# Kernel tuning notes

Hardware: AMD Instinct MI355X
Metric: run time of the kernel (lower is better)

Reference implementation:

```python
import jax, jax.numpy as jnp
import numpy as np

NUM_HEADS = 8


def setup_inputs() -> dict:
    key = jax.random.key(0)
    ks = jax.random.split(key, 5)
    b, c, h, w = 8, 256, 32, 32
    x = jax.random.normal(ks[0], (b, c, h, w), dtype=jnp.float32)
    w_qkv = jax.random.normal(ks[1], (3 * c, c), dtype=jnp.float32) * (c ** -0.5)
    b_qkv = jax.random.normal(ks[2], (3 * c,), dtype=jnp.float32) * 0.02
    w_proj = jax.random.normal(ks[3], (c, c), dtype=jnp.float32) * (c ** -0.5)
    b_proj = jax.random.normal(ks[4], (c,), dtype=jnp.float32) * 0.02
    return {"x": x, "w_qkv": w_qkv, "b_qkv": b_qkv, "w_proj": w_proj, "b_proj": b_proj}


def reference(x, w_qkv, b_qkv, w_proj, b_proj):
    b, c, h, w = x.shape
    nh = NUM_HEADS
    dh = c // nh
    L = h * w
    scale = dh ** -0.5
    # 1x1 conv == per-pixel GEMM
    qkv = jnp.einsum('bchw,oc->bohw', x, w_qkv) + b_qkv[None, :, None, None]
    qkv = qkv.reshape(b, 3, nh, dh, L)
    q, k, v = qkv[:, 0], qkv[:, 1], qkv[:, 2]  # each (b, nh, dh, L)
    attn = jnp.einsum('bhdi,bhdj->bhij', q, k) * scale  # (b, nh, L, L)
    attn = jax.nn.softmax(attn, axis=-1)
    out = jnp.einsum('bhdj,bhij->bhdi', v, attn)  # (b, nh, dh, L)
    out = out.reshape(b, c, h, w)
    proj = jnp.einsum('bchw,oc->bohw', out, w_proj) + b_proj[None, :, None, None]
    return x + proj
```

## Files before the change

kernel.cpp:

```cpp
#include <hip/hip_runtime.h>
#include <math.h>

#define B_   8
#define CIN  256
#define L_   1024
#define NH_  8
#define DH_  32

typedef __attribute__((ext_vector_type(8))) short short8;
typedef __attribute__((ext_vector_type(4))) short short4v;
typedef __attribute__((ext_vector_type(4))) float f32x4;
typedef __attribute__((ext_vector_type(4))) unsigned int uint4v;
typedef __attribute__((ext_vector_type(2))) unsigned int uint2v;

__device__ inline short f2bf_hu(float f) {
    union { float f; unsigned u; } v; v.f = f;
    return (short)((v.u + 0x8000u) >> 16);
}
__device__ inline unsigned pkbf2(float a, float b) {
    union { float f; unsigned u; } x, y; x.f = a; y.f = b;
    return __builtin_amdgcn_perm(y.u + 0x8000u, x.u + 0x8000u, 0x07060302u);
}

__global__ __launch_bounds__(256) void qkv_gemm(
    const float* __restrict__ x, const float* __restrict__ w,
    const float* __restrict__ bias, short* __restrict__ qkvT)
{
    __shared__ short Xs[64][40];
    __shared__ short Wt[128][40];
    const int t = threadIdx.x, lane = t & 63, wv = t >> 6;
    const int n = lane & 15, quad = lane >> 4;
    const int b = blockIdx.z, o0 = blockIdx.y * 128, l0 = blockIdx.x * 64;

    float bias_r[8];
    #pragma unroll
    for (int nf = 0; nf < 8; nf++) bias_r[nf] = bias[o0 + nf * 16 + n];

    f32x4 acc[8];
    #pragma unroll
    for (int nf = 0; nf < 8; nf++) acc[nf] = (f32x4){0.f, 0.f, 0.f, 0.f};

    const int cS = t >> 3, lsS = (t & 7) * 8;

    for (int c0 = 0; c0 < CIN; c0 += 32) {
        {
            const float* xp = &x[(((size_t)b * CIN + c0 + cS) << 10) + l0 + lsS];
            const float4 xa = *(const float4*)xp;
            const float4 xb = *(const float4*)(xp + 4);
            const float vals[8] = {xa.x, xa.y, xa.z, xa.w, xb.x, xb.y, xb.z, xb.w};
            #pragma unroll
            for (int k = 0; k < 8; k++) {
                const int l = lsS + k;
                const int col = (((cS >> 3) ^ (l & 3)) << 3) | (cS & 7);
                Xs[l][col] = f2bf_hu(vals[k]);
            }
        }
        {
            const int o = t >> 1, cs = (t & 1) * 16;
            const float* wp = &w[(size_t)(o0 + o) * CIN + c0 + cs];
            const float4 w0 = *(const float4*)(wp);
            const float4 w1 = *(const float4*)(wp + 4);
            const float4 w2 = *(const float4*)(wp + 8);
            const float4 w3 = *(const float4*)(wp + 12);
            uint4v pa = { pkbf2(w0.x, w0.y), pkbf2(w0.z, w0.w),
                          pkbf2(w1.x, w1.y), pkbf2(w1.z, w1.w) };
            uint4v pb = { pkbf2(w2.x, w2.y), pkbf2(w2.z, w2.w),
                          pkbf2(w3.x, w3.y), pkbf2(w3.z, w3.w) };
            *(uint4v*)&Wt[o][cs]     = pa;
            *(uint4v*)&Wt[o][cs + 8] = pb;
        }
        __syncthreads();

        const int arow = wv * 16 + n;
        const short8 af = *(const short8*)&Xs[arow][(quad ^ (arow & 3)) * 8];
        #pragma unroll
        for (int nf = 0; nf < 8; nf++) {
            const short8 bf = *(const short8*)&Wt[nf * 16 + n][quad * 8];
            acc[nf] = __builtin_amdgcn_mfma_f32_16x16x32_bf16(af, bf, acc[nf], 0, 0, 0);
        }
        __syncthreads();
    }

    #pragma unroll
    for (int reg = 0; reg < 4; reg++) {
        const size_t l = l0 + wv * 16 + quad * 4 + reg;
        short* row = qkvT + (((size_t)b << 10) + l) * 768 + o0 + n;
        #pragma unroll
        for (int nf = 0; nf < 8; nf++)
            row[nf * 16] = f2bf_hu(acc[nf][reg] + bias_r[nf]);
    }
}

__global__ __launch_bounds__(256) void proj_gemm(
    const short* __restrict__ aT, const float* __restrict__ w,
    const float* __restrict__ bias, const float* __restrict__ resid,
    float* __restrict__ out)
{
    __shared__ short Xs[64][40];
    __shared__ short Wt[64][40];
    const int t = threadIdx.x, lane = t & 63, wv = t >> 6;
    const int n = lane & 15, quad = lane >> 4;
    const int b = blockIdx.z, o0 = blockIdx.y * 64, l0 = blockIdx.x * 64;

    float bias_r[4];
    #pragma unroll
    for (int reg = 0; reg < 4; reg++) bias_r[reg] = bias[o0 + wv * 16 + quad * 4 + reg];

    f32x4 acc[4];
    #pragma unroll
    for (int nf = 0; nf < 4; nf++) acc[nf] = (f32x4){0.f, 0.f, 0.f, 0.f};

    for (int c0 = 0; c0 < CIN; c0 += 32) {
        {
            const int l = t >> 2, cs = (t & 3) * 8;
            *(uint4v*)&Xs[l][cs] =
                *(const uint4v*)&aT[(((size_t)b << 10) + l0 + l) * CIN + c0 + cs];
        }
        {
            const int o = t >> 2, cs = (t & 3) * 8;
            const float* wp = &w[(size_t)(o0 + o) * CIN + c0 + cs];
            const float4 a4 = *(const float4*)(wp);
            const float4 b4 = *(const float4*)(wp + 4);
            uint4v pw = { pkbf2(a4.x, a4.y), pkbf2(a4.z, a4.w),
                          pkbf2(b4.x, b4.y), pkbf2(b4.z, b4.w) };
            *(uint4v*)&Wt[o][cs] = pw;
        }
        __syncthreads();

        const short8 af = *(const short8*)&Wt[wv * 16 + n][quad * 8];
        #pragma unroll
        for (int nf = 0; nf < 4; nf++) {
            const short8 bf = *(const short8*)&Xs[nf * 16 + n][quad * 8];
            acc[nf] = __builtin_amdgcn_mfma_f32_16x16x32_bf16(af, bf, acc[nf], 0, 0, 0);
        }
        __syncthreads();
    }

    #pragma unroll
    for (int reg = 0; reg < 4; reg++) {
        const int o = o0 + wv * 16 + quad * 4 + reg;
        #pragma unroll
        for (int nf = 0; nf < 4; nf++) {
            const size_t off = (((size_t)b * CIN + o) << 10) + l0 + nf * 16 + n;
            out[off] = acc[nf][reg] + bias_r[reg] + resid[off];
        }
    }
}

__global__ __launch_bounds__(256) void attn_mfma(
    const short* __restrict__ qkvT, short* __restrict__ attnoT)
{
    __shared__ short Vt[2][32][80];
    __shared__ __align__(16) char umem[64 * 80 * 2];
    short (*Ss)[80] = (short(*)[80])umem;
    float (*OtT)[38] = (float(*)[38])umem;

    const int t = threadIdx.x, lane = t & 63, wv = t >> 6;
    const int n = lane & 15, quad = lane >> 4;
    const int id = blockIdx.x;
    const int bh = id & 63;
    const int b = bh >> 3, h = bh & 7;
    const int i0 = (id >> 6) * 64;

    const short* base = qkvT + ((size_t)b << 10) * 768;

    const short8 qa = *(const short8*)&base[(size_t)(i0 + wv * 16 + n) * 768 + h * DH_ + quad * 8];

    short8 vf2;
    {
        const short one = (n == 0) ? (short)0x3F80 : (short)0;
        #pragma unroll
        for (int u = 0; u < 8; u++) vf2[u] = one;
    }

    f32x4 o_acc[3];
    #pragma unroll
    for (int nf = 0; nf < 3; nf++) o_acc[nf] = (f32x4){0.f, 0.f, 0.f, 0.f};

    const float K1 = 0.25503510f;
    const float K2 = 11.54156036f;
    const int TSTRIDE = 64 * 768;

    const short* kp0 = base + 256 + h * DH_ + (size_t)(0 * 16 + n) * 768 + quad * 8;
    const short* kp1 = kp0 + 16 * 768;
    const short* kp2 = kp0 + 32 * 768;
    const short* kp3 = kp0 + 48 * 768;
    const int jS = t >> 3, dsS = (t & 7) * 4;
    const short* vp0 = base + 512 + h * DH_ + (size_t)jS * 768 + dsS;
    const short* vp1 = vp0 + 32 * 768;

    const int vmsk = ((dsS >> 2) & 7) << 3;
    const int vwo0 = dsS * 80 + (jS ^ vmsk);
    const int vwo1 = dsS * 80 + ((jS + 32) ^ vmsk);
    short* const vtb0 = &Vt[0][0][0];
    short* const vtb1 = &Vt[1][0][0];
    short* const ssw  = &Ss[wv * 16 + n][quad * 4];
    const short* const ssr = &Ss[wv * 16 + n][quad * 8];
    int vro[2][2];
    #pragma unroll
    for (int nf = 0; nf < 2; nf++) {
        const int dv = nf * 16 + n;
        const int msk = ((dv >> 2) & 7) << 3;
        #pragma unroll
        for (int kk = 0; kk < 2; kk++)
            vro[kk][nf] = dv * 80 + ((kk * 32 + quad * 8) ^ msk);
    }

    short8 kfA[4], kfB[4];

    auto stageV = [&](short* vtb) {
        const short4v a = *(const short4v*)vp0; vp0 += TSTRIDE;
        const short4v c = *(const short4v*)vp1; vp1 += TSTRIDE;
        #pragma unroll
        for (int u = 0; u < 4; u++) {
            vtb[vwo0 + u * 80] = a[u];
            vtb[vwo1 + u * 80] = c[u];
        }
    };
    auto loadK = [&](short8* kf) {
        kf[0] = *(const short8*)kp0; kp0 += TSTRIDE;
        kf[1] = *(const short8*)kp1; kp1 += TSTRIDE;
        kf[2] = *(const short8*)kp2; kp2 += TSTRIDE;
        kf[3] = *(const short8*)kp3; kp3 += TSTRIDE;
    };
    auto tile = [&](const short8* kf, const short* vtb) {
        #pragma unroll
        for (int f = 0; f < 4; f++) {
            f32x4 z = {0.f, 0.f, 0.f, 0.f};
            const f32x4 sv = __builtin_amdgcn_mfma_f32_16x16x32_bf16(kf[f], qa, z, 0, 0, 0);
            const float p0 = __builtin_amdgcn_exp2f(fmaf(sv[0], K1, -K2));
            const float p1 = __builtin_amdgcn_exp2f(fmaf(sv[1], K1, -K2));
            const float p2 = __builtin_amdgcn_exp2f(fmaf(sv[2], K1, -K2));
            const float p3 = __builtin_amdgcn_exp2f(fmaf(sv[3], K1, -K2));
            uint2v pk = { pkbf2(p0, p1), pkbf2(p2, p3) };
            *(uint2v*)(ssw + f * 16) = pk;
        }
        #pragma unroll
        for (int kk = 0; kk < 2; kk++) {
            const short8 pf = *(const short8*)(ssr + kk * 32);
            #pragma unroll
            for (int nf = 0; nf < 2; nf++) {
                const short8 vf = *(const short8*)(vtb + vro[kk][nf]);
                o_acc[nf] = __builtin_amdgcn_mfma_f32_16x16x32_bf16(pf, vf, o_acc[nf], 0, 0, 0);
            }
            o_acc[2] = __builtin_amdgcn_mfma_f32_16x16x32_bf16(pf, vf2, o_acc[2], 0, 0, 0);
        }
    };

    stageV(vtb0);
    loadK(kfA);

    for (int itp = 0; itp < 8; itp++) {
        __syncthreads();
        stageV(vtb1);
        loadK(kfB);
        tile(kfA, vtb0);
        __syncthreads();
        if (itp < 7) { stageV(vtb0); loadK(kfA); }
        tile(kfB, vtb1);
    }

    __syncthreads();
    #pragma unroll
    for (int r = 0; r < 4; r++) {
        const float lv  = __shfl(o_acc[2][r], lane & 48, 64);
        const float inv = 1.f / lv;
        const int il = wv * 16 + quad * 4 + r;
        OtT[il][n]      = o_acc[0][r] * inv;
        OtT[il][16 + n] = o_acc[1][r] * inv;
    }
    __syncthreads();
    short* ob = attnoT + (((size_t)b << 10) + i0) * CIN + h * DH_;
    #pragma unroll
    for (int r = 0; r < 2; r++) {
        const int idx = t + r * 256;
        const int l = idx >> 3, cs = (idx & 7) * 4;
        uint2v pv;
        pv.x = pkbf2(OtT[l][cs],     OtT[l][cs + 1]);
        pv.y = pkbf2(OtT[l][cs + 2], OtT[l][cs + 3]);
        *(uint2v*)&ob[(size_t)l * CIN + cs] = pv;
    }
}

extern "C" void kernel_launch(void* const* d_in, const int* in_sizes, int n_in,
                              void* d_out, int out_size, void* d_ws, size_t ws_size,
                              hipStream_t stream) {
    const float* x      = (const float*)d_in[0];
    const float* w_qkv  = (const float*)d_in[1];
    const float* b_qkv  = (const float*)d_in[2];
    const float* w_proj = (const float*)d_in[3];
    const float* b_proj = (const float*)d_in[4];
    float* out = (float*)d_out;

    short* qkvT   = (short*)d_ws;
    short* attnoT = qkvT + (size_t)B_ * L_ * 768;

    qkv_gemm<<<dim3(16, 6, B_), 256, 0, stream>>>(x, w_qkv, b_qkv, qkvT);
    attn_mfma<<<dim3(1024), 256, 0, stream>>>(qkvT, attnoT);
    proj_gemm<<<dim3(16, 4, B_), 256, 0, stream>>>(attnoT, w_proj, b_proj, x, out);
}
```

Baseline: 127.5 us.

## Process two query sub-tiles per wave in attention to reuse K/V tiles

Each attention block now covers 128 query rows instead of 64: every wave holds two Q fragments and two sets of output accumulators, and the grid is halved to 512 blocks. Each K fragment loaded from global memory and each V tile staged in LDS now feeds twice as many MFMAs, so K/V traffic and staging cost per query are halved. The Ss buffer grows with a padded row stride of 88. The trade-off is higher register and LDS use per block and fewer blocks, which may reduce occupancy and the ability to hide latency on a 256-CU device.

```diff
diff --git a/kernel.cpp b/kernel.cpp
--- a/kernel.cpp
+++ b/kernel.cpp
@@ -151,8 +151,8 @@
     const short* __restrict__ qkvT, short* __restrict__ attnoT)
 {
     __shared__ short Vt[2][32][80];
-    __shared__ __align__(16) char umem[64 * 80 * 2];
-    short (*Ss)[80] = (short(*)[80])umem;
+    __shared__ __align__(16) char umem[128 * 88 * 2];
+    short (*Ss)[88] = (short(*)[88])umem;
     float (*OtT)[38] = (float(*)[38])umem;
 
     const int t = threadIdx.x, lane = t & 63, wv = t >> 6;
@@ -160,11 +160,15 @@
     const int id = blockIdx.x;
     const int bh = id & 63;
     const int b = bh >> 3, h = bh & 7;
-    const int i0 = (id >> 6) * 64;
+    const int i0 = (id >> 6) * 128;
 
     const short* base = qkvT + ((size_t)b << 10) * 768;
 
-    const short8 qa = *(const short8*)&base[(size_t)(i0 + wv * 16 + n) * 768 + h * DH_ + quad * 8];
+    short8 qa[2];
+    #pragma unroll
+    for (int a = 0; a < 2; a++)
+        qa[a] = *(const short8*)&base[(size_t)(i0 + wv * 32 + a * 16 + n) * 768
+                                      + h * DH_ + quad * 8];
 
     short8 vf2;
     {
@@ -173,15 +177,17 @@
         for (int u = 0; u < 8; u++) vf2[u] = one;
     }
 
-    f32x4 o_acc[3];
-    #pragma unroll
-    for (int nf = 0; nf < 3; nf++) o_acc[nf] = (f32x4){0.f, 0.f, 0.f, 0.f};
+    f32x4 o_acc[2][3];
+    #pragma unroll
+    for (int a = 0; a < 2; a++)
+        #pragma unroll
+        for (int nf = 0; nf < 3; nf++) o_acc[a][nf] = (f32x4){0.f, 0.f, 0.f, 0.f};
 
     const float K1 = 0.25503510f;
     const float K2 = 11.54156036f;
     const int TSTRIDE = 64 * 768;
 
-    const short* kp0 = base + 256 + h * DH_ + (size_t)(0 * 16 + n) * 768 + quad * 8;
+    const short* kp0 = base + 256 + h * DH_ + (size_t)n * 768 + quad * 8;
     const short* kp1 = kp0 + 16 * 768;
     const short* kp2 = kp0 + 32 * 768;
     const short* kp3 = kp0 + 48 * 768;
@@ -194,8 +200,8 @@
     const int vwo1 = dsS * 80 + ((jS + 32) ^ vmsk);
     short* const vtb0 = &Vt[0][0][0];
     short* const vtb1 = &Vt[1][0][0];
-    short* const ssw  = &Ss[wv * 16 + n][quad * 4];
-    const short* const ssr = &Ss[wv * 16 + n][quad * 8];
+    short* const ssw  = &Ss[wv * 32 + n][quad * 4];
+    const short* const ssr = &Ss[wv * 32 + n][quad * 8];
     int vro[2][2];
     #pragma unroll
     for (int nf = 0; nf < 2; nf++) {
@@ -226,24 +232,34 @@
     auto tile = [&](const short8* kf, const short* vtb) {
         #pragma unroll
         for (int f = 0; f < 4; f++) {
-            f32x4 z = {0.f, 0.f, 0.f, 0.f};
-            const f32x4 sv = __builtin_amdgcn_mfma_f32_16x16x32_bf16(kf[f], qa, z, 0, 0, 0);
-            const float p0 = __builtin_amdgcn_exp2f(fmaf(sv[0], K1, -K2));
-            const float p1 = __builtin_amdgcn_exp2f(fmaf(sv[1], K1, -K2));
-            const float p2 = __builtin_amdgcn_exp2f(fmaf(sv[2], K1, -K2));
-            const float p3 = __builtin_amdgcn_exp2f(fmaf(sv[3], K1, -K2));
-            uint2v pk = { pkbf2(p0, p1), pkbf2(p2, p3) };
-            *(uint2v*)(ssw + f * 16) = pk;
+            #pragma unroll
+            for (int a = 0; a < 2; a++) {
+                f32x4 z = {0.f, 0.f, 0.f, 0.f};
+                const f32x4 sv = __builtin_amdgcn_mfma_f32_16x16x32_bf16(kf[f], qa[a], z, 0, 0, 0);
+                const float p0 = __builtin_amdgcn_exp2f(fmaf(sv[0], K1, -K2));
+                const float p1 = __builtin_amdgcn_exp2f(fmaf(sv[1], K1, -K2));
+                const float p2 = __builtin_amdgcn_exp2f(fmaf(sv[2], K1, -K2));
+                const float p3 = __builtin_amdgcn_exp2f(fmaf(sv[3], K1, -K2));
+                uint2v pk = { pkbf2(p0, p1), pkbf2(p2, p3) };
+                *(uint2v*)(ssw + a * 16 * 88 + f * 16) = pk;
+            }
         }
         #pragma unroll
         for (int kk = 0; kk < 2; kk++) {
-            const short8 pf = *(const short8*)(ssr + kk * 32);
+            short8 pf[2];
+            #pragma unroll
+            for (int a = 0; a < 2; a++)
+                pf[a] = *(const short8*)(ssr + a * 16 * 88 + kk * 32);
             #pragma unroll
             for (int nf = 0; nf < 2; nf++) {
                 const short8 vf = *(const short8*)(vtb + vro[kk][nf]);
-                o_acc[nf] = __builtin_amdgcn_mfma_f32_16x16x32_bf16(pf, vf, o_acc[nf], 0, 0, 0);
+                #pragma unroll
+                for (int a = 0; a < 2; a++)
+                    o_acc[a][nf] = __builtin_amdgcn_mfma_f32_16x16x32_bf16(pf[a], vf, o_acc[a][nf], 0, 0, 0);
             }
-            o_acc[2] = __builtin_amdgcn_mfma_f32_16x16x32_bf16(pf, vf2, o_acc[2], 0, 0, 0);
+            #pragma unroll
+            for (int a = 0; a < 2; a++)
+                o_acc[a][2] = __builtin_amdgcn_mfma_f32_16x16x32_bf16(pf[a], vf2, o_acc[a][2], 0, 0, 0);
         }
     };
 
@@ -262,17 +278,19 @@
 
     __syncthreads();
     #pragma unroll
-    for (int r = 0; r < 4; r++) {
-        const float lv  = __shfl(o_acc[2][r], lane & 48, 64);
-        const float inv = 1.f / lv;
-        const int il = wv * 16 + quad * 4 + r;
-        OtT[il][n]      = o_acc[0][r] * inv;
-        OtT[il][16 + n] = o_acc[1][r] * inv;
-    }
+    for (int a = 0; a < 2; a++)
+        #pragma unroll
+        for (int r = 0; r < 4; r++) {
+            const float lv  = __shfl(o_acc[a][2][r], lane & 48, 64);
+            const float inv = 1.f / lv;
+            const int il = wv * 32 + a * 16 + quad * 4 + r;
+            OtT[il][n]      = o_acc[a][0][r] * inv;
+            OtT[il][16 + n] = o_acc[a][1][r] * inv;
+        }
     __syncthreads();
     short* ob = attnoT + (((size_t)b << 10) + i0) * CIN + h * DH_;
     #pragma unroll
-    for (int r = 0; r < 2; r++) {
+    for (int r = 0; r < 4; r++) {
         const int idx = t + r * 256;
         const int l = idx >> 3, cs = (idx & 7) * 4;
         uint2v pv;
@@ -296,6 +314,6 @@
     short* attnoT = qkvT + (size_t)B_ * L_ * 768;
 
     qkv_gemm<<<dim3(16, 6, B_), 256, 0, stream>>>(x, w_qkv, b_qkv, qkvT);
-    attn_mfma<<<dim3(1024), 256, 0, stream>>>(qkvT, attnoT);
+    attn_mfma<<<dim3(512), 256, 0, stream>>>(qkvT, attnoT);
     proj_gemm<<<dim3(16, 4, B_), 256, 0, stream>>>(attnoT, w_proj, b_proj, x, out);
 }
```

After: 115.7 us. 9.2% less time.
